# Optimization experiments

Hardware: AMD Instinct MI355X
Metric: run time of the kernel (lower is better)

The kernel has to match this reference:

```python
import jax, jax.numpy as jnp
import numpy as np


def _gru_dir(x, wih, whh, bih, bhh):
    # x: [B, T, Din]; torch GRU gate order is (r, z, n)
    H = whh.shape[-1]
    def step(h, xt):
        gi = xt @ wih.T + bih            # [B, 3H]
        gh = h @ whh.T + bhh             # [B, 3H]
        i_r, i_z, i_n = jnp.split(gi, 3, axis=-1)
        h_r, h_z, h_n = jnp.split(gh, 3, axis=-1)
        r = jax.nn.sigmoid(i_r + h_r)
        z = jax.nn.sigmoid(i_z + h_z)
        n = jnp.tanh(i_n + r * h_n)
        h = (1.0 - z) * n + z * h
        return h, h
    h0 = jnp.zeros((x.shape[0], H), x.dtype)
    _, ys = jax.lax.scan(step, h0, jnp.swapaxes(x, 0, 1))
    return jnp.swapaxes(ys, 0, 1)


def _bigru(x, wih, whh, bih, bhh):
    f = _gru_dir(x, wih[0], whh[0], bih[0], bhh[0])
    b = _gru_dir(x[:, ::-1], wih[1], whh[1], bih[1], bhh[1])[:, ::-1]
    return jnp.concatenate([f, b], axis=-1)


def _masked_max(h, lens):
    # max over first lens[i] timesteps; zeros when lens[i] == 0 (matches max_pool1d loop)
    T = h.shape[1]
    mask = (jnp.arange(T)[None, :] < lens[:, None])[..., None]
    pooled = jnp.max(jnp.where(mask, h, -jnp.inf), axis=1)
    return jnp.where((lens > 0)[:, None], pooled, 0.0)


def _forward(x, events, n_docs, event_tfs, sent_targets, embed,
             word_wih, word_whh, word_bih, word_bhh,
             sent_wih, sent_whh, sent_bih, sent_bhh,
             doc_wih, doc_whh, doc_bih, doc_bhh,
             ev_wih, ev_whh, ev_bih, ev_bhh,
             doc_pos_embed, sent_pos_embed,
             w_event_content, W_event_sal, event_tf, event_sent, event_bias,
             w_sent_content, W_sent_sal, w_sent_doc_pos, w_sent_pos,
             W_event_rel, b_event_rel, event_para, event_zero, sent_bias):
    S, T = x.shape
    spd = S // n_docs                  # sentences per doc (uniform doc_lens)
    eps = events.shape[0] // S         # events per sentence (uniform event_sent_lens)
    sent_lens = jnp.sum(jnp.sign(x), axis=1)
    # embed_frozen=True -> detach embedding output
    xw = jax.lax.stop_gradient(embed[x])               # [S, T, D]
    h = _bigru(xw, word_wih, word_whh, word_bih, word_bhh)  # [S, T, 2H]
    sent_vec = _masked_max(h, sent_lens)               # [S, 2H]
    # sent_RNN per doc (state resets per doc) then full-length max pool
    dh = _bigru(sent_vec.reshape(n_docs, spd, -1), sent_wih, sent_whh, sent_bih, sent_bhh)
    doc_vec = jnp.max(dh, axis=1)                      # [n_docs, 2H]
    bh = _bigru(doc_vec[None], doc_wih, doc_whh, doc_bih, doc_bhh)
    blog_vec = jnp.max(bh[0], axis=0)                  # [2H]
    # teacher_forcing=1.0 -> first-pass sent scores are the detached targets
    sent_probs0 = jax.lax.stop_gradient(sent_targets)
    # events: fixed length 4, full max pool
    eh = _bigru(jax.lax.stop_gradient(embed[events]), ev_wih, ev_whh, ev_bih, ev_bhh)
    event_vec = jnp.max(eh, axis=1)                    # [E, 2H]
    event_sum = jnp.mean(event_vec, axis=0)            # [2H] (avg pool over all events)
    abs_idx = jnp.repeat(jnp.arange(S), eps)           # event -> absolute sentence index
    ec = event_vec @ w_event_content                   # [E]
    es = jnp.einsum('ed,df,f->e', event_vec, W_event_sal, event_sum)
    event_probs = ec + event_tf[0] * event_tfs + event_bias[0] + es + event_sent[0] * sent_probs0[abs_idx]
    event_scores = jax.lax.stop_gradient(event_probs)
    # per-sentence event relevance (Bilinear with bias, dotted with detached scores)
    ev3 = event_vec.reshape(S, eps, -1)
    sc3 = event_scores.reshape(S, eps)
    sim = jnp.einsum('sd,df,sef->se', sent_vec, W_event_rel, ev3) + b_event_rel[0]
    event_rel = event_para[0] * jnp.sum(sim * sc3, axis=1)   # [S]
    doc_idx = jnp.repeat(jnp.arange(n_docs), spd)
    context = jnp.concatenate([jnp.broadcast_to(blog_vec, (S, blog_vec.shape[0])), doc_vec[doc_idx]], axis=1)  # [S, 4H]
    s_content = sent_vec @ w_sent_content
    s_sal = jnp.einsum('sd,df,sf->s', sent_vec, W_sent_sal, context)
    PD = doc_pos_embed.shape[0]
    PS = sent_pos_embed.shape[0]
    dpos = (doc_idx * PD) // n_docs                    # int(i * pos_doc_size / doc_num)
    j_idx = jnp.tile(jnp.arange(spd), n_docs)
    spos = (j_idx * PS) // spd                         # int(j * pos_sent_size / doc_lens[i])
    s_dpos = doc_pos_embed[dpos] @ w_sent_doc_pos
    s_pos = sent_pos_embed[spos] @ w_sent_pos
    sent_out = s_content + s_sal + s_dpos + s_pos + event_rel + sent_bias[0]
    return sent_out, event_probs


def setup_inputs() -> dict:
    key = jax.random.key(0)
    ks = jax.random.split(key, 40)
    V, D, H, P = 50000, 300, 256, 50
    PD, PS = 40, 30
    n_docs, spd, T, eps = 32, 32, 32, 3
    S = n_docs * spd
    E = S * eps
    def rn(k, shape, s=0.05):
        return jax.random.normal(k, shape, jnp.float32) * s
    inp = {}
    inp['x'] = jax.random.randint(ks[0], (S, T), 0, V, jnp.int32)
    inp['events'] = jax.random.randint(ks[1], (E, 4), 1, V, jnp.int32)
    inp['doc_lens'] = jnp.full((n_docs,), spd, jnp.int32)
    inp['event_doc_lens'] = jnp.full((n_docs,), spd * eps, jnp.int32)
    inp['event_sent_lens'] = jnp.full((S,), eps, jnp.int32)
    inp['event_tfs'] = jax.random.uniform(ks[2], (E,), jnp.float32)
    inp['event_targets'] = jax.random.uniform(ks[3], (E,), jnp.float32)
    inp['sent_targets'] = jax.random.uniform(ks[4], (S,), jnp.float32)
    inp['embed'] = rn(ks[5], (V, D), 0.1)
    i = 6
    for name, din in [('word', D), ('sent', 2 * H), ('doc', 2 * H), ('ev', D)]:
        inp[name + '_wih'] = rn(ks[i], (2, 3 * H, din)); i += 1
        inp[name + '_whh'] = rn(ks[i], (2, 3 * H, H)); i += 1
        inp[name + '_bih'] = rn(ks[i], (2, 3 * H)); i += 1
        inp[name + '_bhh'] = rn(ks[i], (2, 3 * H)); i += 1
    inp['doc_pos_embed'] = rn(ks[i], (PD, P), 0.1); i += 1
    inp['sent_pos_embed'] = rn(ks[i], (PS, P), 0.1); i += 1
    inp['w_event_content'] = rn(ks[i], (2 * H,)); i += 1
    inp['W_event_sal'] = rn(ks[i], (2 * H, 2 * H)); i += 1
    inp['event_tf'] = rn(ks[i], (1,)); i += 1
    inp['event_sent'] = rn(ks[i], (1,)); i += 1
    inp['event_bias'] = rn(ks[i], (1,)); i += 1
    inp['w_sent_content'] = rn(ks[i], (2 * H,)); i += 1
    inp['W_sent_sal'] = rn(ks[i], (2 * H, 4 * H)); i += 1
    inp['w_sent_doc_pos'] = rn(ks[i], (P,)); i += 1
    inp['w_sent_pos'] = rn(ks[i], (P,)); i += 1
    inp['W_event_rel'] = rn(ks[i], (2 * H, 2 * H)); i += 1
    inp['b_event_rel'] = rn(ks[i], (1,)); i += 1
    inp['event_para'] = rn(ks[i], (1,)); i += 1
    inp['event_zero'] = rn(ks[i], (1,)); i += 1
    inp['sent_bias'] = rn(ks[i], (1,)); i += 1
    return inp


def reference(x, events, doc_lens, event_doc_lens, event_sent_lens, event_tfs, event_targets, sent_targets, embed,
              word_wih, word_whh, word_bih, word_bhh,
              sent_wih, sent_whh, sent_bih, sent_bhh,
              doc_wih, doc_whh, doc_bih, doc_bhh,
              ev_wih, ev_whh, ev_bih, ev_bhh,
              doc_pos_embed, sent_pos_embed,
              w_event_content, W_event_sal, event_tf, event_sent, event_bias,
              w_sent_content, W_sent_sal, w_sent_doc_pos, w_sent_pos,
              W_event_rel, b_event_rel, event_para, event_zero, sent_bias):
    n_docs = doc_lens.shape[0]
    return _forward(x, events, n_docs, event_tfs, sent_targets, embed,
                    word_wih, word_whh, word_bih, word_bhh,
                    sent_wih, sent_whh, sent_bih, sent_bhh,
                    doc_wih, doc_whh, doc_bih, doc_bhh,
                    ev_wih, ev_whh, ev_bih, ev_bhh,
                    doc_pos_embed, sent_pos_embed,
                    w_event_content, W_event_sal, event_tf, event_sent, event_bias,
                    w_sent_content, W_sent_sal, w_sent_doc_pos, w_sent_pos,
                    W_event_rel, b_event_rel, event_para, event_zero, sent_bias)
```

## Files before the change

kernel.cpp:

```cpp
#include <hip/hip_runtime.h>
#include <hip/hip_bf16.h>
#include <math.h>

typedef __bf16 bf16_t;
typedef __bf16 bf16x8 __attribute__((ext_vector_type(8)));
typedef __bf16 bf16x4 __attribute__((ext_vector_type(4)));
typedef float  f32x4  __attribute__((ext_vector_type(4)));

#define S_TOT 1024
#define T_W   32
#define D_EMB 300
#define KP    320
#define G3    768
#define Hh    256
#define H2    512
#define E_TOT 3072
#define NCANON 33

__device__ __forceinline__ float fsigm(float x) {
  float e = __builtin_amdgcn_exp2f(x * -1.4426950408889634f);
  return __builtin_amdgcn_rcpf(1.f + e);
}
__device__ __forceinline__ float ftanh_(float x) {
  float e = __builtin_amdgcn_exp2f(x * 2.8853900817779268f);
  return 1.f - 2.f * __builtin_amdgcn_rcpf(1.f + e);
}

__global__ void k_detect(const unsigned short* __restrict__ w, int* __restrict__ flag) {
  int lane = threadIdx.x;
  int sane = 0;
  for (int i = lane; i < 256; i += 64) {
    unsigned short v = w[2 * i];
    int ex = (v >> 7) & 0xFF;
    sane += (ex >= 96 && ex <= 134) ? 1 : 0;
  }
  #pragma unroll
  for (int o = 32; o > 0; o >>= 1) sane += __shfl_down(sane, o, 64);
  if (lane == 0) flag[0] = (sane >= 128) ? 1 : 0;
}

struct Canon {
  const void* src[NCANON];
  int off[NCANON + 1];
};
__global__ void k_canon(Canon c, const int* __restrict__ flag, float* __restrict__ dst) {
  int i = blockIdx.x * 256 + threadIdx.x;
  if (i >= c.off[NCANON]) return;
  int seg = 0;
  while (c.off[seg + 1] <= i) ++seg;
  int j = i - c.off[seg];
  dst[i] = flag[0] ? (float)((const bf16_t*)c.src[seg])[j]
                   : ((const float*)c.src[seg])[j];
}

struct PrepArgs {
  const float* whh[4];   bf16_t* pk[4];
  const float* wih2[2];  bf16_t* pw2[2];
  const float* bih4[4];  const float* bhh4[4]; float* bc4[4];
  const float* tsrc[2];  float* tdst[2];
  const int* x; int* lens;
};
__global__ __launch_bounds__(256) void k_prep(PrepArgs a) {
  int b = blockIdx.x, tid = threadIdx.x;
  if (b < 768) {
    int ti = b / 192, lb = b % 192;
    int id = lb * 256 + tid;
    int lane = id & 63;
    int k0 = (id >> 6) & 7;
    int t9 = id >> 9;
    int sl = t9 % 6;
    int wb = t9 / 6;
    int wv = wb & 7;
    int dir = wb >> 3;
    int g = sl >> 1, jt = sl & 1;
    int l16 = lane & 15, quad = lane >> 4;
    int n = g * Hh + wv * 32 + jt * 16 + l16;
    const float* src = a.whh[ti] + ((size_t)dir * G3 + n) * Hh + k0 * 32 + quad * 8;
    bf16_t* dst = a.pk[ti] + (size_t)id * 8;
    #pragma unroll
    for (int i = 0; i < 8; ++i) dst[i] = (bf16_t)src[i];
  } else if (b < 1248) {
    int ti = (b - 768) / 240, lb = (b - 768) % 240;
    int id = lb * 256 + tid;
    int lane = id & 63;
    int su = id >> 6;
    int s  = su % 40;
    int n0 = (su / 40) % 12;
    int dir = su / 480;
    int j = s / 10, k0 = s % 10;
    int l16 = lane & 15, quad = lane >> 4;
    int n = n0 * 64 + j * 16 + l16;
    int c = k0 * 32 + quad * 8;
    const float* src = a.wih2[ti] + ((size_t)dir * G3 + n) * D_EMB + c;
    bf16_t* dst = a.pw2[ti] + (size_t)id * 8;
    #pragma unroll
    for (int i = 0; i < 8; ++i)
      dst[i] = (c + i < D_EMB) ? (bf16_t)src[i] : (bf16_t)0.f;
  } else if (b < 1272) {
    int ti = (b - 1248) / 6, lb = (b - 1248) % 6;
    int i = lb * 256 + tid;
    if (i < 2 * G3) {
      int c = i % G3;
      a.bc4[ti][i] = a.bih4[ti][i] + (c < 2 * Hh ? a.bhh4[ti][i] : 0.f);
    }
  } else if (b < 2808) {
    __shared__ float tile[32][33];
    int lb = b - 1272;
    int which = lb / 768;
    int r = lb % 768;
    int bx = r % 24, by = (r / 24) % 16, d = r / 384;
    const float* w = a.tsrc[which];
    float* out = a.tdst[which];
    int n0 = bx * 32, k0 = by * 32;
    int tx = tid & 31, ty = tid >> 5;
    for (int i = ty; i < 32; i += 8)
      tile[i][tx] = w[((size_t)d * G3 + n0 + i) * H2 + k0 + tx];
    __syncthreads();
    for (int i = ty; i < 32; i += 8)
      out[((size_t)d * H2 + k0 + i) * G3 + n0 + tx] = tile[tx][i];
  } else {
    int s = (b - 2808) * 256 + tid;
    if (s < S_TOT) {
      int c = 0;
      for (int t = 0; t < T_W; ++t) c += (a.x[s * T_W + t] != 0) ? 1 : 0;
      a.lens[s] = c;
    }
  }
}

__device__ __forceinline__ void gib_body(
    const int* __restrict__ toks, const void* __restrict__ embed,
    const bf16_t* __restrict__ wpk_base, const float* __restrict__ bih_base,
    const int* __restrict__ flag, bf16_t* __restrict__ gi_base,
    size_t gi_dstride, int mbase, int bx) {
  __shared__ __align__(16) bf16_t Bt[2][20480];
  int tid = threadIdx.x;
  int wave = tid >> 6, lane = tid & 63;
  int l16 = lane & 15, quad = lane >> 4;
  int m0 = bx * 128;
  int dir = blockIdx.y;
  int isb = flag[0];
  const bf16_t* wpk = wpk_base + (size_t)dir * 245760;
  const float*  bih = bih_base + (size_t)dir * G3;
  bf16_t* gi = gi_base + (size_t)dir * gi_dstride;

  bf16x8 ah[10], al[10];
  {
    int tok = toks[mbase + m0 + wave * 16 + l16];
    if (isb) {
      const bf16_t* er = (const bf16_t*)embed + (size_t)tok * D_EMB;
      #pragma unroll
      for (int k0 = 0; k0 < 10; ++k0) {
        int c = k0 * 32 + quad * 8;
        bf16x8 v = {};
        if (c + 8 <= D_EMB) {
          bf16x4 t0 = *(const bf16x4*)(er + c);
          bf16x4 t1 = *(const bf16x4*)(er + c + 4);
          v[0]=t0[0]; v[1]=t0[1]; v[2]=t0[2]; v[3]=t0[3];
          v[4]=t1[0]; v[5]=t1[1]; v[6]=t1[2]; v[7]=t1[3];
        } else if (c < D_EMB) {
          bf16x4 t0 = *(const bf16x4*)(er + c);
          v[0]=t0[0]; v[1]=t0[1]; v[2]=t0[2]; v[3]=t0[3];
        }
        ah[k0] = v;
        al[k0] = (bf16x8){};
      }
    } else {
      const float* er = (const float*)embed + (size_t)tok * D_EMB;
      #pragma unroll
      for (int k0 = 0; k0 < 10; ++k0) {
        int c = k0 * 32 + quad * 8;
        float v[8];
        #pragma unroll
// ... 50 lines not shown
        for (int j = 0; j < 4; ++j)
          acc[j] = __builtin_amdgcn_mfma_f32_16x16x32_bf16(al[k0], b[j], acc[j], 0, 0, 0);
        #pragma unroll
        for (int j = 0; j < 4; ++j)
          acc[j] = __builtin_amdgcn_mfma_f32_16x16x32_bf16(ah[k0], b[j], acc[j], 0, 0, 0);
      }
    }
    {
      int row0 = m0 + wave * 16 + quad * 4;
      #pragma unroll
      for (int j = 0; j < 4; ++j) {
        int col = n0 * 64 + j * 16 + l16;
        float bb = bih[col];
        #pragma unroll
        for (int rr = 0; rr < 4; ++rr)
          gi[(size_t)(row0 + rr) * G3 + col] = (bf16_t)(acc[j][rr] + bb);
      }
    }
    if (n0 + 1 < 12) {
      bf16_t* dst = &Bt[cur ^ 1][tid * 8];
      #pragma unroll
      for (int i = 0; i < 5; ++i) *(bf16x8*)(dst + i * 4096) = stg[i];
      __syncthreads();
    }
  }
}

__global__ __launch_bounds__(512, 1) void k_giB(
    const int* __restrict__ toks, const void* __restrict__ embed,
    const bf16_t* __restrict__ wpk_base, const float* __restrict__ bih_base,
    const int* __restrict__ flag, bf16_t* __restrict__ gi_base,
    size_t gi_dstride, int mbase) {
  gib_body(toks, embed, wpk_base, bih_base, flag, gi_base, gi_dstride, mbase,
           blockIdx.x);
}

__device__ __forceinline__ void dev_sgemm(
    const float* __restrict__ A, const float* __restrict__ B,
    const float* __restrict__ bias, void* __restrict__ C,
    int M, int N, int K, int obf, int bx, int by) {
  __shared__ float As[32][65];
  __shared__ float Bs[32][65];
  int bm = bx * 64, bn = by * 64;
  int tid = threadIdx.x;
  int tx = tid & 15, ty = tid >> 4;
  float acc[4][4] = {};
  for (int k0 = 0; k0 < K; k0 += 32) {
    for (int i = tid; i < 64 * 32; i += 256) {
      int m = i >> 5, k = i & 31;
      As[k][m] = (bm + m < M) ? A[(size_t)(bm + m) * K + k0 + k] : 0.f;
    }
    for (int i = tid; i < 32 * 64; i += 256) {
      int k = i >> 6, n = i & 63;
      Bs[k][n] = B[(size_t)(k0 + k) * N + bn + n];
    }
    __syncthreads();
    #pragma unroll 8
    for (int k = 0; k < 32; ++k) {
      float a[4], b[4];
      #pragma unroll
      for (int i = 0; i < 4; ++i) a[i] = As[k][ty + i * 16];
      #pragma unroll
      for (int j = 0; j < 4; ++j) b[j] = Bs[k][tx + j * 16];
      #pragma unroll
      for (int i = 0; i < 4; ++i)
        #pragma unroll
        for (int j = 0; j < 4; ++j) acc[i][j] += a[i] * b[j];
    }
    __syncthreads();
  }
  for (int i = 0; i < 4; ++i) {
    int m = bm + ty + i * 16;
    if (m >= M) continue;
    for (int j = 0; j < 4; ++j) {
      int n = bn + tx + j * 16;
      float v = acc[i][j] + (bias ? bias[n] : 0.f);
      if (obf) ((bf16_t*)C)[(size_t)m * N + n] = (bf16_t)v;
      else     ((float*)C)[(size_t)m * N + n] = v;
    }
  }
}

__global__ __launch_bounds__(256) void k_sgemm_su(
    const float* __restrict__ sv, const float* __restrict__ wSt,
    const float* __restrict__ bcS, bf16_t* __restrict__ sgi,
    const float* __restrict__ wer, float* __restrict__ u) {
  int y = blockIdx.y;
  if (y < 12)
    dev_sgemm(sv, wSt, bcS, sgi, 1024, G3, H2, 1, blockIdx.x, y);
  else if (y < 24)
    dev_sgemm(sv, wSt + (size_t)H2 * G3, bcS + G3, sgi + (size_t)S_TOT * G3,
              1024, G3, H2, 1, blockIdx.x, y - 12);
  else
    dev_sgemm(sv, wer, nullptr, u, 1024, H2, H2, 0, blockIdx.x, y - 24);
}

__global__ __launch_bounds__(256) void k_sgemm_d(
    const float* __restrict__ dv, const float* __restrict__ wDt,
    const float* __restrict__ bcD, bf16_t* __restrict__ dgi) {
  int y = blockIdx.y;
  if (y < 12)
    dev_sgemm(dv, wDt, bcD, dgi, 32, G3, H2, 1, 0, y);
  else
    dev_sgemm(dv, wDt + (size_t)H2 * G3, bcD + G3, dgi + (size_t)32 * G3,
              32, G3, H2, 1, 0, y - 12);
}

__device__ __forceinline__ void gru_body(
    const bf16_t* __restrict__ gi, size_t gi_dstride,
    const bf16_t* __restrict__ whhP, const float* __restrict__ bhh,
    const int* __restrict__ lens, float* __restrict__ pool,
    int T, int sbase, int nsent, int sblk) {
  int dir = blockIdx.y;
  int tid = threadIdx.x;
  int wave = tid >> 6, lane = tid & 63;
  int l16 = lane & 15, quad = lane >> 4;
  const bf16_t* giD  = gi + (size_t)dir * gi_dstride;
  const float*  bhhD = bhh + (size_t)dir * G3;

  __shared__ __align__(16) bf16_t hA[2][8][16][4][8];

  bf16x8 Bf[48];
  {
    const bf16_t* Bb = whhP + (size_t)dir * G3 * Hh + (size_t)wave * 48 * 512 + lane * 8;
    #pragma unroll
    for (int s = 0; s < 48; ++s) Bf[s] = *(const bf16x8*)(Bb + s * 512);
  }
  float bhn[2];
  #pragma unroll
  for (int jt = 0; jt < 2; ++jt)
    bhn[jt] = bhhD[2 * Hh + wave * 32 + jt * 16 + l16];
  int Lm[4];
  #pragma unroll
  for (int r = 0; r < 4; ++r) {
    int sa = sblk + quad * 4 + r;
    Lm[r] = (lens && sa < nsent) ? lens[sbase + sa] : T;
  }
  float pmax[2][4], hreg[2][4];
  #pragma unroll
  for (int jt = 0; jt < 2; ++jt)
    #pragma unroll
    for (int r = 0; r < 4; ++r) { pmax[jt][r] = -1e30f; hreg[jt][r] = 0.f; }

  int t0 = dir ? (T - 1) : 0;
  long long stepoff = dir ? -(long long)G3 : (long long)G3;
  const bf16_t* rp[4];
// ... 63 lines not shown
        for (int r = 0; r < 4; ++r) {
          gv[0][jt][r] = rp[r][j];
          gv[1][jt][r] = rp[r][Hh + j];
          gv[2][jt][r] = rp[r][2 * Hh + j];
        }
      }
    }
    asm volatile("s_waitcnt lgkmcnt(0)" ::: "memory");
    __builtin_amdgcn_s_barrier();
    cur ^= 1;
  }
  #pragma unroll
  for (int jt = 0; jt < 2; ++jt) {
    int j = wave * 32 + jt * 16 + l16;
    #pragma unroll
    for (int r = 0; r < 4; ++r) {
      int sa = sblk + quad * 4 + r;
      if (sa < nsent) {
        float v = pmax[jt][r];
        if (v < -9e29f) v = 0.f;
        pool[(size_t)(sbase + sa) * H2 + dir * Hh + j] = v;
      }
    }
  }
}

__global__ __launch_bounds__(512)
__attribute__((amdgpu_waves_per_eu(2, 2)))
void k_gruM(
    const bf16_t* __restrict__ gi, size_t gi_dstride,
    const bf16_t* __restrict__ whhP, const float* __restrict__ bhh,
    const int* __restrict__ lens, float* __restrict__ pool,
    int T, int sbase, int nsent) {
  gru_body(gi, gi_dstride, whhP, bhh, lens, pool, T, sbase, nsent, blockIdx.x * 16);
}

__global__ __launch_bounds__(512)
__attribute__((amdgpu_waves_per_eu(2, 2)))
void k_wg(
    const bf16_t* __restrict__ giW, size_t strideW,
    const bf16_t* __restrict__ whhW, const float* __restrict__ bhhW,
    const int* __restrict__ lens, float* __restrict__ poolW,
    const int* __restrict__ etoks, const void* __restrict__ embed,
    const bf16_t* __restrict__ wpkE, const float* __restrict__ bihE,
    const int* __restrict__ flag, bf16_t* __restrict__ giE, size_t strideE) {
  if ((int)blockIdx.x < 64)
    gru_body(giW, strideW, whhW, bhhW, lens, poolW, 32, 0, 1024,
             blockIdx.x * 16);
  else
    gib_body(etoks, embed, wpkE, bihE, flag, giE, strideE, 0,
             blockIdx.x - 64);
}

__global__ __launch_bounds__(512) void k_colsal(
    const float* __restrict__ ev, float* __restrict__ part,
    const float* __restrict__ W, const float* __restrict__ blog,
    const float* __restrict__ dv, float* __restrict__ wsal) {
  int b = blockIdx.x, t = threadIdx.x;
  if (b < 48) {
    int r0 = b * 64;
    float s = 0.f;
    for (int r = 0; r < 64; ++r) s += ev[(size_t)(r0 + r) * H2 + t];
    part[(size_t)b * H2 + t] = s;
  } else {
    int doc = b - 48;
    const float* row = W + (size_t)t * (2 * H2);
    const float* dvr = dv + (size_t)doc * H2;
    float s = 0.f;
    for (int f = 0; f < H2; ++f) s += row[f] * blog[f];
    for (int f = 0; f < H2; ++f) s += row[H2 + f] * dvr[f];
    wsal[(size_t)doc * H2 + t] = s;
  }
}

__global__ __launch_bounds__(512) void k_esumves(
    const float* __restrict__ part, const float* __restrict__ W,
    float* __restrict__ ves) {
  __shared__ float es[H2];
  int t = threadIdx.x;
  float s = 0.f;
  for (int b = 0; b < 48; ++b) s += part[(size_t)b * H2 + t];
  es[t] = s;
  __syncthreads();
  const float* row = W + (size_t)t * H2;
  float v = 0.f;
  for (int f = 0; f < H2; ++f) v += row[f] * es[f];
  ves[t] = v * (1.f / 3072.f);
}

__global__ __launch_bounds__(256) void k_eventprobs(
    const float* __restrict__ evv, const float* __restrict__ ves,
    const float* __restrict__ w_ec, const float* __restrict__ tfs,
    const float* __restrict__ st, const float* __restrict__ c_tf,
    const float* __restrict__ c_sent, const float* __restrict__ c_bias,
    const int* __restrict__ flag, float* __restrict__ probs, void* __restrict__ outp) {
  int lane = threadIdx.x & 63;
  int e = blockIdx.x * 4 + (threadIdx.x >> 6);
  const float* row = evv + (size_t)e * H2;
  float s = 0.f;
  for (int f = lane; f < H2; f += 64) s += row[f] * (w_ec[f] + ves[f]);
  #pragma unroll
  for (int o = 32; o > 0; o >>= 1) s += __shfl_down(s, o, 64);
  if (lane == 0) {
    float p = s + c_tf[0] * tfs[e] + c_bias[0] + c_sent[0] * st[e / 3];
    probs[e] = p;
    if (flag[0]) ((bf16_t*)outp)[S_TOT + e] = (bf16_t)p;
    else         ((float*)outp)[S_TOT + e] = p;
  }
}

__global__ __launch_bounds__(256) void k_sentout(
    const float* __restrict__ sv, const float* __restrict__ u,
    const float* __restrict__ evv, const float* __restrict__ probs,
    const float* __restrict__ wsal, const float* __restrict__ w_sc,
    const float* __restrict__ dpe, const float* __restrict__ spe,
    const float* __restrict__ w_sdp, const float* __restrict__ w_sp,
    const float* __restrict__ b_rel, const float* __restrict__ para,
    const float* __restrict__ sbias, const int* __restrict__ flag,
    void* __restrict__ outp) {
  int lane = threadIdx.x & 63;
  int s = blockIdx.x * 4 + (threadIdx.x >> 6);
  int doc = s >> 5, jj = s & 31;
  const float* svr = sv + (size_t)s * H2;
  const float* ur  = u + (size_t)s * H2;
  const float* wd  = wsal + (size_t)doc * H2;
  float acc = 0.f, e0 = 0.f, e1 = 0.f, e2 = 0.f;
  for (int f = lane; f < H2; f += 64) {
    float svf = svr[f], uf = ur[f];
    acc += svf * (w_sc[f] + wd[f]);
    e0 += uf * evv[(size_t)(s * 3 + 0) * H2 + f];
    e1 += uf * evv[(size_t)(s * 3 + 1) * H2 + f];
    e2 += uf * evv[(size_t)(s * 3 + 2) * H2 + f];
  }
  if (lane < 50) {
    int dpos = (doc * 40) / 32;
    int spos = (jj * 30) / 32;
    acc += dpe[dpos * 50 + lane] * w_sdp[lane] + spe[spos * 50 + lane] * w_sp[lane];
  }
  #pragma unroll
  for (int o = 32; o > 0; o >>= 1) {
    acc += __shfl_down(acc, o, 64);
    e0  += __shfl_down(e0, o, 64);
    e1  += __shfl_down(e1, o, 64);
    e2  += __shfl_down(e2, o, 64);
  }
  if (lane == 0) {
    float br = b_rel[0];
    float rel = (e0 + br) * probs[s * 3 + 0] + (e1 + br) * probs[s * 3 + 1]
              + (e2 + br) * probs[s * 3 + 2];
    float v = acc + para[0] * rel + sbias[0];
    if (flag[0]) ((bf16_t*)outp)[s] = (bf16_t)v;
    else         ((float*)outp)[s] = v;
  }
}

extern "C" void kernel_launch(void* const* d_in, const int* in_sizes, int n_in,
                              void* d_out, int out_size, void* d_ws, size_t ws_size,
                              hipStream_t stream) {
  (void)in_sizes; (void)n_in; (void)out_size;
  const int* x      = (const int*)d_in[0];
  const int* events = (const int*)d_in[1];
  const void* embed = d_in[8];

  char* ws = (char*)d_ws;
  size_t off = 0;
  auto alloc = [&](size_t bytes) -> void* {
    void* p = ws + off;
    off += (bytes + 255) & ~(size_t)255;
    return p;
  };

  static const int cidx[NCANON] = {9,10,11,12, 13,14,15,16, 17,18,19,20, 21,22,23,24,
                                   25,26,27,28,29,30,31, 32,33,34,35, 36,37,38,40, 5,7};
  static const int csz[NCANON]  = {2*G3*D_EMB, 2*G3*Hh, 2*G3, 2*G3,
                                   2*G3*H2,    2*G3*Hh, 2*G3, 2*G3,
                                   2*G3*H2,    2*G3*Hh, 2*G3, 2*G3,
                                   2*G3*D_EMB, 2*G3*Hh, 2*G3, 2*G3,
                                   40*50, 30*50, H2, H2*H2, 1, 1, 1,
                                   H2, H2*2*H2, 50, 50,
                                   H2*H2, 1, 1, 1, E_TOT, S_TOT};
  Canon cd;
  int tot = 0;
  for (int i = 0; i < NCANON; ++i) { cd.src[i] = d_in[cidx[i]]; cd.off[i] = tot; tot += csz[i]; }
  cd.off[NCANON] = tot;

  int*   flag  = (int*)alloc(256);
  float* canon = (float*)alloc((size_t)tot * 4);
  float* cptr[NCANON];
  for (int i = 0; i < NCANON; ++i) cptr[i] = canon + cd.off[i];
  float *cw_wih = cptr[0], *cw_whh = cptr[1], *cw_bih = cptr[2], *cw_bhh = cptr[3];
  float *cs_wih = cptr[4], *cs_whh = cptr[5], *cs_bih = cptr[6], *cs_bhh = cptr[7];
  float *cd_wih = cptr[8], *cd_whh = cptr[9], *cd_bih = cptr[10], *cd_bhh = cptr[11];
  float *ce_wih = cptr[12], *ce_whh = cptr[13], *ce_bih = cptr[14], *ce_bhh = cptr[15];
  float *c_dpe = cptr[16], *c_spe = cptr[17], *c_wec = cptr[18], *c_Wes = cptr[19];
  float *c_tf = cptr[20], *c_sent = cptr[21], *c_ebias = cptr[22];
  float *c_wsc = cptr[23], *c_Wss = cptr[24], *c_wsdp = cptr[25], *c_wsp = cptr[26];
  float *c_Wer = cptr[27], *c_brel = cptr[28], *c_para = cptr[29], *c_sbias = cptr[30];
  float *c_tfs = cptr[31], *c_starg = cptr[32];

  bf16_t* packW = (bf16_t*)alloc((size_t)2 * G3 * Hh * 2);
  bf16_t* packE = (bf16_t*)alloc((size_t)2 * G3 * Hh * 2);
  bf16_t* packS = (bf16_t*)alloc((size_t)2 * G3 * Hh * 2);
  bf16_t* packD = (bf16_t*)alloc((size_t)2 * G3 * Hh * 2);
  bf16_t* packGiW = (bf16_t*)alloc((size_t)2 * 12 * 40 * 64 * 8 * 2);
  bf16_t* packGiE = (bf16_t*)alloc((size_t)2 * 12 * 40 * 64 * 8 * 2);
  float*  bcW  = (float*)alloc((size_t)2 * G3 * 4);
  float*  bcE  = (float*)alloc((size_t)2 * G3 * 4);
  float*  bcS  = (float*)alloc((size_t)2 * G3 * 4);
  float*  bcD  = (float*)alloc((size_t)2 * G3 * 4);
  float*  sv   = (float*)alloc((size_t)S_TOT * H2 * 4);
  float*  evv  = (float*)alloc((size_t)E_TOT * H2 * 4);
  float*  dv   = (float*)alloc((size_t)32 * H2 * 4);
  float*  blog = (float*)alloc((size_t)H2 * 4);
  float*  wSt  = (float*)alloc((size_t)2 * H2 * G3 * 4);
  float*  wDt  = (float*)alloc((size_t)2 * H2 * G3 * 4);
  float*  u    = (float*)alloc((size_t)S_TOT * H2 * 4);
  float*  part = (float*)alloc((size_t)48 * H2 * 4);
  float*  ves  = (float*)alloc((size_t)H2 * 4);
  float*  wsal = (float*)alloc((size_t)32 * H2 * 4);
  float*  probs= (float*)alloc((size_t)E_TOT * 4);
  int*    lens = (int*)alloc((size_t)S_TOT * 4);
  bf16_t* sgi  = (bf16_t*)alloc((size_t)2 * S_TOT * G3 * 2);
  bf16_t* dgi  = (bf16_t*)alloc((size_t)2 * 32 * G3 * 2);

  size_t fixed = off;
  size_t avail = (ws_size > fixed) ? (ws_size - fixed) : 0;
  const size_t needW = (size_t)2 * 32768 * G3 * 2;
  const size_t needE = (size_t)2 * 12288 * G3 * 2;
  bf16_t* gib = (bf16_t*)(ws + fixed);

  PrepArgs pa;
  pa.whh[0]=cw_whh; pa.whh[1]=ce_whh; pa.whh[2]=cs_whh; pa.whh[3]=cd_whh;
  pa.pk[0]=packW; pa.pk[1]=packE; pa.pk[2]=packS; pa.pk[3]=packD;
  pa.wih2[0]=cw_wih; pa.wih2[1]=ce_wih; pa.pw2[0]=packGiW; pa.pw2[1]=packGiE;
  pa.bih4[0]=cw_bih; pa.bih4[1]=ce_bih; pa.bih4[2]=cs_bih; pa.bih4[3]=cd_bih;
  pa.bhh4[0]=cw_bhh; pa.bhh4[1]=ce_bhh; pa.bhh4[2]=cs_bhh; pa.bhh4[3]=cd_bhh;
  pa.bc4[0]=bcW; pa.bc4[1]=bcE; pa.bc4[2]=bcS; pa.bc4[3]=bcD;
  pa.tsrc[0]=cs_wih; pa.tsrc[1]=cd_wih; pa.tdst[0]=wSt; pa.tdst[1]=wDt;
  pa.x = x; pa.lens = lens;

  k_detect<<<1, 64, 0, stream>>>((const unsigned short*)embed, flag);
  k_canon<<<(tot + 255) / 256, 256, 0, stream>>>(cd, flag, canon);
  k_prep<<<2812, 256, 0, stream>>>(pa);

  if (avail >= needW + needE) {
    bf16_t* egib = (bf16_t*)((char*)gib + ((needW + 255) & ~(size_t)255));
    k_giB<<<dim3(256, 2), 512, 0, stream>>>(x, embed, packGiW, bcW, flag,
                                            gib, (size_t)32768 * G3, 0);
    k_wg<<<dim3(64 + 96, 2), 512, 0, stream>>>(
        gib, (size_t)32768 * G3, packW, cw_bhh, lens, sv,
        events, embed, packGiE, bcE, flag, egib, (size_t)12288 * G3);
    k_gruM<<<dim3(192, 2), 512, 0, stream>>>(
        egib, (size_t)12288 * G3, packE, ce_bhh, nullptr, evv, 4, 0, 3072);
  } else {
    long long rpc = (long long)(avail / ((size_t)G3 * 2 * 2));
    rpc &= ~511LL;
    if (rpc < 512) rpc = 512;
    if (rpc > 32768) rpc = 32768;
    for (long long r0 = 0; r0 < 32768; r0 += rpc) {
      long long rows = 32768 - r0; if (rows > rpc) rows = rpc;
      k_giB<<<dim3((int)(rows / 128), 2), 512, 0, stream>>>(
          x, embed, packGiW, bcW, flag, gib, (size_t)rows * G3, (int)r0);
      k_gruM<<<dim3((int)(rows / 512), 2), 512, 0, stream>>>(
          gib, (size_t)rows * G3, packW, cw_bhh, lens, sv, 32, (int)(r0 / 32),
          (int)(rows / 32));
    }
    for (long long r0 = 0; r0 < 12288; r0 += rpc) {
      long long rows = 12288 - r0; if (rows > rpc) rows = rpc;
      k_giB<<<dim3((int)(rows / 128), 2), 512, 0, stream>>>(
          events, embed, packGiE, bcE, flag, gib, (size_t)rows * G3, (int)r0);
      k_gruM<<<dim3((int)(rows / 64), 2), 512, 0, stream>>>(
          gib, (size_t)rows * G3, packE, ce_bhh, nullptr, evv, 4, (int)(r0 / 4),
          (int)(rows / 4));
    }
  }

  k_sgemm_su<<<dim3(16, 32), 256, 0, stream>>>(sv, wSt, bcS, sgi, c_Wer, u);
  k_gruM<<<dim3(2, 2), 512, 0, stream>>>(sgi, (size_t)S_TOT * G3, packS, cs_bhh,
                                         nullptr, dv, 32, 0, 32);
  k_sgemm_d<<<dim3(1, 24), 256, 0, stream>>>(dv, wDt, bcD, dgi);
  k_gruM<<<dim3(1, 2), 512, 0, stream>>>(dgi, (size_t)32 * G3, packD, cd_bhh,
                                         nullptr, blog, 32, 0, 1);
  k_colsal<<<80, 512, 0, stream>>>(evv, part, c_Wss, blog, dv, wsal);
  k_esumves<<<1, 512, 0, stream>>>(part, c_Wes, ves);
  k_eventprobs<<<768, 256, 0, stream>>>(evv, ves, c_wec, c_tfs, c_starg,
                                        c_tf, c_sent, c_ebias, flag, probs, d_out);
  k_sentout<<<256, 256, 0, stream>>>(sv, u, evv, probs, wsal, c_wsc, c_dpe, c_spe,
                                     c_wsdp, c_wsp, c_brel, c_para, c_sbias, flag, d_out);
}
```

Measured before the change: 913.0 us.

## Fuse tail kernels into combined launches and drop big-weight canonicalization pass

Removes the separate canonicalization kernel for large GRU weights; the prep kernel now reads raw fp32/bf16 inputs directly and handles the small canonical tensors itself. The tail-stage kernels are regrouped so independent work runs in shared launches: the event GRU with the sentence GEMMs, the sentence GRU with the column sums, the doc GEMM with the event-sum projection, and the doc GRU with the event probabilities. This reduces launch count and serialization and lets small, latency-bound stages overlap. The cost is heterogeneous blocks within a launch and forced occupancy hints that may not suit every branch.

```diff
diff --git a/kernel.cpp b/kernel.cpp
--- a/kernel.cpp
+++ b/kernel.cpp
@@ -10,12 +10,11 @@
 #define S_TOT 1024
 #define T_W   32
 #define D_EMB 300
-#define KP    320
 #define G3    768
 #define Hh    256
 #define H2    512
 #define E_TOT 3072
-#define NCANON 33
+#define NC2   21
 
 __device__ __forceinline__ float fsigm(float x) {
   float e = __builtin_amdgcn_exp2f(x * -1.4426950408889634f);
@@ -24,6 +23,9 @@
 __device__ __forceinline__ float ftanh_(float x) {
   float e = __builtin_amdgcn_exp2f(x * 2.8853900817779268f);
   return 1.f - 2.f * __builtin_amdgcn_rcpf(1.f + e);
+}
+__device__ __forceinline__ float ldf(const void* p, size_t i, int isb) {
+  return isb ? (float)((const bf16_t*)p)[i] : ((const float*)p)[i];
 }
 
 __global__ void k_detect(const unsigned short* __restrict__ w, int* __restrict__ flag) {
@@ -40,28 +42,21 @@
 }
 
 struct Canon {
-  const void* src[NCANON];
-  int off[NCANON + 1];
+  const void* src[NC2];
+  int off[NC2 + 1];
 };
-__global__ void k_canon(Canon c, const int* __restrict__ flag, float* __restrict__ dst) {
-  int i = blockIdx.x * 256 + threadIdx.x;
-  if (i >= c.off[NCANON]) return;
-  int seg = 0;
-  while (c.off[seg + 1] <= i) ++seg;
-  int j = i - c.off[seg];
-  dst[i] = flag[0] ? (float)((const bf16_t*)c.src[seg])[j]
-                   : ((const float*)c.src[seg])[j];
-}
-
 struct PrepArgs {
-  const float* whh[4];   bf16_t* pk[4];
-  const float* wih2[2];  bf16_t* pw2[2];
-  const float* bih4[4];  const float* bhh4[4]; float* bc4[4];
-  const float* tsrc[2];  float* tdst[2];
+  const void* whhR[4];  bf16_t* pk[4];
+  const void* wihR[2];  bf16_t* pw2[2];
+  const void* bihR[4];  const void* bhhR[4]; float* bc4[4];
+  const void* tsrcR[2]; float* tdst[2];
   const int* x; int* lens;
+  const int* flag;
+  Canon c; float* canon_dst; int tot2;
 };
-__global__ __launch_bounds__(256) void k_prep(PrepArgs a) {
+__global__ __launch_bounds__(256) void k_prepAll(PrepArgs a) {
   int b = blockIdx.x, tid = threadIdx.x;
+  int isb = a.flag[0];
   if (b < 768) {
     int ti = b / 192, lb = b % 192;
     int id = lb * 256 + tid;
@@ -75,10 +70,10 @@
     int g = sl >> 1, jt = sl & 1;
     int l16 = lane & 15, quad = lane >> 4;
     int n = g * Hh + wv * 32 + jt * 16 + l16;
-    const float* src = a.whh[ti] + ((size_t)dir * G3 + n) * Hh + k0 * 32 + quad * 8;
+    size_t base = ((size_t)dir * G3 + n) * Hh + k0 * 32 + quad * 8;
     bf16_t* dst = a.pk[ti] + (size_t)id * 8;
     #pragma unroll
-    for (int i = 0; i < 8; ++i) dst[i] = (bf16_t)src[i];
+    for (int i = 0; i < 8; ++i) dst[i] = (bf16_t)ldf(a.whhR[ti], base + i, isb);
   } else if (b < 1248) {
     int ti = (b - 768) / 240, lb = (b - 768) % 240;
     int id = lb * 256 + tid;
@@ -91,17 +86,17 @@
     int l16 = lane & 15, quad = lane >> 4;
     int n = n0 * 64 + j * 16 + l16;
     int c = k0 * 32 + quad * 8;
-    const float* src = a.wih2[ti] + ((size_t)dir * G3 + n) * D_EMB + c;
+    size_t base = ((size_t)dir * G3 + n) * D_EMB + c;
     bf16_t* dst = a.pw2[ti] + (size_t)id * 8;
     #pragma unroll
     for (int i = 0; i < 8; ++i)
-      dst[i] = (c + i < D_EMB) ? (bf16_t)src[i] : (bf16_t)0.f;
+      dst[i] = (c + i < D_EMB) ? (bf16_t)ldf(a.wihR[ti], base + i, isb) : (bf16_t)0.f;
   } else if (b < 1272) {
     int ti = (b - 1248) / 6, lb = (b - 1248) % 6;
     int i = lb * 256 + tid;
     if (i < 2 * G3) {
       int c = i % G3;
-      a.bc4[ti][i] = a.bih4[ti][i] + (c < 2 * Hh ? a.bhh4[ti][i] : 0.f);
+      a.bc4[ti][i] = ldf(a.bihR[ti], i, isb) + (c < 2 * Hh ? ldf(a.bhhR[ti], i, isb) : 0.f);
     }
   } else if (b < 2808) {
     __shared__ float tile[32][33];
@@ -109,22 +104,31 @@
     int which = lb / 768;
     int r = lb % 768;
     int bx = r % 24, by = (r / 24) % 16, d = r / 384;
-    const float* w = a.tsrc[which];
+    const void* w = a.tsrcR[which];
     float* out = a.tdst[which];
     int n0 = bx * 32, k0 = by * 32;
     int tx = tid & 31, ty = tid >> 5;
     for (int i = ty; i < 32; i += 8)
-      tile[i][tx] = w[((size_t)d * G3 + n0 + i) * H2 + k0 + tx];
+      tile[i][tx] = ldf(w, ((size_t)d * G3 + n0 + i) * H2 + k0 + tx, isb);
     __syncthreads();
     for (int i = ty; i < 32; i += 8)
       out[((size_t)d * H2 + k0 + i) * G3 + n0 + tx] = tile[tx][i];
-  } else {
+  } else if (b < 2812) {
     int s = (b - 2808) * 256 + tid;
     if (s < S_TOT) {
       int c = 0;
       for (int t = 0; t < T_W; ++t) c += (a.x[s * T_W + t] != 0) ? 1 : 0;
       a.lens[s] = c;
     }
+  } else {
+    int i = (b - 2812) * 256 + tid;
+    if (i < a.tot2) {
+      int seg = 0;
+      while (a.c.off[seg + 1] <= i) ++seg;
+      int j = i - a.c.off[seg];
+      a.canon_dst[i] = isb ? (float)((const bf16_t*)a.c.src[seg])[j]
+                           : ((const float*)a.c.src[seg])[j];
+    }
   }
 }
 
@@ -132,13 +136,12 @@
     const int* __restrict__ toks, const void* __restrict__ embed,
     const bf16_t* __restrict__ wpk_base, const float* __restrict__ bih_base,
     const int* __restrict__ flag, bf16_t* __restrict__ gi_base,
-    size_t gi_dstride, int mbase, int bx) {
+    size_t gi_dstride, int mbase, int bx, int dir) {
   __shared__ __align__(16) bf16_t Bt[2][20480];
   int tid = threadIdx.x;
   int wave = tid >> 6, lane = tid & 63;
   int l16 = lane & 15, quad = lane >> 4;
   int m0 = bx * 128;
-  int dir = blockIdx.y;
   int isb = flag[0];
   const bf16_t* wpk = wpk_base + (size_t)dir * 245760;
   const float*  bih = bih_base + (size_t)dir * G3;
@@ -255,7 +258,7 @@
     const int* __restrict__ flag, bf16_t* __restrict__ gi_base,
     size_t gi_dstride, int mbase) {
   gib_body(toks, embed, wpk_base, bih_base, flag, gi_base, gi_dstride, mbase,
-           blockIdx.x);
+           blockIdx.x, blockIdx.y);
 }
 
 __device__ __forceinline__ void dev_sgemm(
@@ -304,37 +307,61 @@
   }
 }
 
-__global__ __launch_bounds__(256) void k_sgemm_su(
-    const float* __restrict__ sv, const float* __restrict__ wSt,
-    const float* __restrict__ bcS, bf16_t* __restrict__ sgi,
-    const float* __restrict__ wer, float* __restrict__ u) {
-  int y = blockIdx.y;
-  if (y < 12)
-    dev_sgemm(sv, wSt, bcS, sgi, 1024, G3, H2, 1, blockIdx.x, y);
-  else if (y < 24)
-    dev_sgemm(sv, wSt + (size_t)H2 * G3, bcS + G3, sgi + (size_t)S_TOT * G3,
-              1024, G3, H2, 1, blockIdx.x, y - 12);
-  else
-    dev_sgemm(sv, wer, nullptr, u, 1024, H2, H2, 0, blockIdx.x, y - 24);
-}
-
-__global__ __launch_bounds__(256) void k_sgemm_d(
-    const float* __restrict__ dv, const float* __restrict__ wDt,
-    const float* __restrict__ bcD, bf16_t* __restrict__ dgi) {
-  int y = blockIdx.y;
-  if (y < 12)
-    dev_sgemm(dv, wDt, bcD, dgi, 32, G3, H2, 1, 0, y);
-  else
-    dev_sgemm(dv, wDt + (size_t)H2 * G3, bcD + G3, dgi + (size_t)32 * G3,
-              32, G3, H2, 1, 0, y - 12);
+__device__ __forceinline__ void dev_sgemm512(
+    const float* __restrict__ A, const float* __restrict__ B,
+    const float* __restrict__ bias, void* __restrict__ C,
+    int M, int N, int K, int obf, int bx, int by) {
+  __shared__ float As[32][65];
+  __shared__ float Bs[32][65];
+  int bm = bx * 64, bn = by * 64;
+  int tid = threadIdx.x;
+  int tx = tid & 15, ty = (tid >> 4) & 15;
+  float acc[4][4] = {};
+  for (int k0 = 0; k0 < K; k0 += 32) {
+    for (int i = tid; i < 64 * 32; i += 512) {
+      int m = i >> 5, k = i & 31;
+      As[k][m] = (bm + m < M) ? A[(size_t)(bm + m) * K + k0 + k] : 0.f;
+    }
+    for (int i = tid; i < 32 * 64; i += 512) {
+      int k = i >> 6, n = i & 63;
+      Bs[k][n] = B[(size_t)(k0 + k) * N + bn + n];
+    }
+    __syncthreads();
+    if (tid < 256) {
+      #pragma unroll 8
+      for (int k = 0; k < 32; ++k) {
+        float a[4], b[4];
+        #pragma unroll
+        for (int i = 0; i < 4; ++i) a[i] = As[k][ty + i * 16];
+        #pragma unroll
+        for (int j = 0; j < 4; ++j) b[j] = Bs[k][tx + j * 16];
+        #pragma unroll
+        for (int i = 0; i < 4; ++i)
+          #pragma unroll
+          for (int j = 0; j < 4; ++j) acc[i][j] += a[i] * b[j];
+      }
+    }
+    __syncthreads();
+  }
+  if (tid < 256) {
+    for (int i = 0; i < 4; ++i) {
+      int m = bm + ty + i * 16;
+      if (m >= M) continue;
+      for (int j = 0; j < 4; ++j) {
+        int n = bn + tx + j * 16;
+        float v = acc[i][j] + (bias ? bias[n] : 0.f);
+        if (obf) ((bf16_t*)C)[(size_t)m * N + n] = (bf16_t)v;
+        else     ((float*)C)[(size_t)m * N + n] = v;
+      }
+    }
+  }
 }
 
 __device__ __forceinline__ void gru_body(
     const bf16_t* __restrict__ gi, size_t gi_dstride,
     const bf16_t* __restrict__ whhP, const float* __restrict__ bhh,
     const int* __restrict__ lens, float* __restrict__ pool,
-    int T, int sbase, int nsent, int sblk) {
-  int dir = blockIdx.y;
+    int T, int sbase, int nsent, int sblk, int dir) {
   int tid = threadIdx.x;
   int wave = tid >> 6, lane = tid & 63;
   int l16 = lane & 15, quad = lane >> 4;
@@ -464,7 +491,8 @@
     const bf16_t* __restrict__ whhP, const float* __restrict__ bhh,
     const int* __restrict__ lens, float* __restrict__ pool,
     int T, int sbase, int nsent) {
-  gru_body(gi, gi_dstride, whhP, bhh, lens, pool, T, sbase, nsent, blockIdx.x * 16);
+  gru_body(gi, gi_dstride, whhP, bhh, lens, pool, T, sbase, nsent,
+           blockIdx.x * 16, blockIdx.y);
 }
 
 __global__ __launch_bounds__(512)
@@ -478,67 +506,128 @@
     const int* __restrict__ flag, bf16_t* __restrict__ giE, size_t strideE) {
   if ((int)blockIdx.x < 64)
     gru_body(giW, strideW, whhW, bhhW, lens, poolW, 32, 0, 1024,
-             blockIdx.x * 16);
+             blockIdx.x * 16, blockIdx.y);
   else
     gib_body(etoks, embed, wpkE, bihE, flag, giE, strideE, 0,
-             blockIdx.x - 64);
-}
-
-__global__ __launch_bounds__(512) void k_colsal(
-    const float* __restrict__ ev, float* __restrict__ part,
-    const float* __restrict__ W, const float* __restrict__ blog,
-    const float* __restrict__ dv, float* __restrict__ wsal) {
+             blockIdx.x - 64, blockIdx.y);
+}
+
+__global__ __launch_bounds__(512)
+__attribute__((amdgpu_waves_per_eu(2, 2)))
+void k_tail1(
+    const bf16_t* __restrict__ giE, size_t strideE,
+    const bf16_t* __restrict__ packE, const float* __restrict__ bhhE,
+    float* __restrict__ evv,
+    const float* __restrict__ sv, const float* __restrict__ wSt,
+    const float* __restrict__ bcS, bf16_t* __restrict__ sgi,
+    const float* __restrict__ wer, float* __restrict__ u, int evblocks) {
+  int b = blockIdx.x;
+  if (b < evblocks) {
+    int dir = b / 192, bx = b % 192;
+    gru_body(giE, strideE, packE, bhhE, nullptr, evv, 4, 0, 3072, bx * 16, dir);
+  } else {
+    int b2 = b - evblocks;
+    int bx = b2 & 15, y = b2 >> 4;
+    if (y < 12)
+      dev_sgemm512(sv, wSt, bcS, sgi, 1024, G3, H2, 1, bx, y);
+    else if (y < 24)
+      dev_sgemm512(sv, wSt + (size_t)H2 * G3, bcS + G3, sgi + (size_t)S_TOT * G3,
+                   1024, G3, H2, 1, bx, y - 12);
+    else
+      dev_sgemm512(sv, wer, nullptr, u, 1024, H2, H2, 0, bx, y - 24);
+  }
+}
+
+__global__ __launch_bounds__(512)
+__attribute__((amdgpu_waves_per_eu(2, 2)))
+void k_tail2(
+    const bf16_t* __restrict__ sgi, const bf16_t* __restrict__ packS,
+    const float* __restrict__ bhhS, float* __restrict__ dv,
+    const float* __restrict__ evv, float* __restrict__ part) {
   int b = blockIdx.x, t = threadIdx.x;
-  if (b < 48) {
-    int r0 = b * 64;
+  if (b < 4) {
+    gru_body(sgi, (size_t)S_TOT * G3, packS, bhhS, nullptr, dv, 32, 0, 32,
+             (b & 1) * 16, b >> 1);
+  } else {
+    int cb = b - 4;
+    int r0 = cb * 64;
     float s = 0.f;
-    for (int r = 0; r < 64; ++r) s += ev[(size_t)(r0 + r) * H2 + t];
-    part[(size_t)b * H2 + t] = s;
+    for (int r = 0; r < 64; ++r) s += evv[(size_t)(r0 + r) * H2 + t];
+    part[(size_t)cb * H2 + t] = s;
+  }
+}
+
+__global__ __launch_bounds__(256) void k_tail3(
+    const float* __restrict__ dv, const float* __restrict__ wDt,
+    const float* __restrict__ bcD, bf16_t* __restrict__ dgi,
+    const float* __restrict__ part, const float* __restrict__ Wes,
+    float* __restrict__ ves) {
+  int b = blockIdx.x, t = threadIdx.x;
+  if (b < 24) {
+    int y = b;
+    if (y < 12)
+      dev_sgemm(dv, wDt, bcD, dgi, 32, G3, H2, 1, 0, y);
+    else
+      dev_sgemm(dv, wDt + (size_t)H2 * G3, bcD + G3, dgi + (size_t)32 * G3,
+                32, G3, H2, 1, 0, y - 12);
   } else {
-    int doc = b - 48;
-    const float* row = W + (size_t)t * (2 * H2);
-    const float* dvr = dv + (size_t)doc * H2;
-    float s = 0.f;
-    for (int f = 0; f < H2; ++f) s += row[f] * blog[f];
-    for (int f = 0; f < H2; ++f) s += row[H2 + f] * dvr[f];
-    wsal[(size_t)doc * H2 + t] = s;
-  }
-}
-
-__global__ __launch_bounds__(512) void k_esumves(
-    const float* __restrict__ part, const float* __restrict__ W,
-    float* __restrict__ ves) {
-  __shared__ float es[H2];
-  int t = threadIdx.x;
-  float s = 0.f;
-  for (int b = 0; b < 48; ++b) s += part[(size_t)b * H2 + t];
-  es[t] = s;
-  __syncthreads();
-  const float* row = W + (size_t)t * H2;
-  float v = 0.f;
-  for (int f = 0; f < H2; ++f) v += row[f] * es[f];
-  ves[t] = v * (1.f / 3072.f);
-}
-
-__global__ __launch_bounds__(256) void k_eventprobs(
+    __shared__ float es[H2];
+    for (int c = t; c < H2; c += 256) {
+      float s = 0.f;
+      for (int bb = 0; bb < 48; ++bb) s += part[(size_t)bb * H2 + c];
+      es[c] = s;
+    }
+    __syncthreads();
+    for (int r = t; r < H2; r += 256) {
+      const float* row = Wes + (size_t)r * H2;
+      float v = 0.f;
+      for (int f = 0; f < H2; ++f) v += row[f] * es[f];
+      ves[r] = v * (1.f / 3072.f);
+    }
+  }
+}
+
+__global__ __launch_bounds__(512)
+__attribute__((amdgpu_waves_per_eu(2, 2)))
+void k_tail4(
+    const bf16_t* __restrict__ dgi, const bf16_t* __restrict__ packD,
+    const float* __restrict__ bhhD, float* __restrict__ blog,
     const float* __restrict__ evv, const float* __restrict__ ves,
     const float* __restrict__ w_ec, const float* __restrict__ tfs,
     const float* __restrict__ st, const float* __restrict__ c_tf,
     const float* __restrict__ c_sent, const float* __restrict__ c_bias,
-    const int* __restrict__ flag, float* __restrict__ probs, void* __restrict__ outp) {
-  int lane = threadIdx.x & 63;
-  int e = blockIdx.x * 4 + (threadIdx.x >> 6);
-  const float* row = evv + (size_t)e * H2;
+    const int* __restrict__ flag, float* __restrict__ probs,
+    void* __restrict__ outp) {
+  int b = blockIdx.x;
+  if (b < 2) {
+    gru_body(dgi, (size_t)32 * G3, packD, bhhD, nullptr, blog, 32, 0, 1, 0, b);
+  } else {
+    int lane = threadIdx.x & 63;
+    int e = (b - 2) * 8 + (threadIdx.x >> 6);
+    const float* row = evv + (size_t)e * H2;
+    float s = 0.f;
+    for (int f = lane; f < H2; f += 64) s += row[f] * (w_ec[f] + ves[f]);
+    #pragma unroll
+    for (int o = 32; o > 0; o >>= 1) s += __shfl_down(s, o, 64);
+    if (lane == 0) {
+      float p = s + c_tf[0] * tfs[e] + c_bias[0] + c_sent[0] * st[e / 3];
+      probs[e] = p;
+      if (flag[0]) ((bf16_t*)outp)[S_TOT + e] = (bf16_t)p;
+      else         ((float*)outp)[S_TOT + e] = p;
+    }
+  }
+}
+
+__global__ __launch_bounds__(512) void k_tail5(
+    const float* __restrict__ W, const float* __restrict__ blog,
+    const float* __restrict__ dv, float* __restrict__ wsal) {
+  int doc = blockIdx.x, t = threadIdx.x;
+  const float* row = W + (size_t)t * (2 * H2);
+  const float* dvr = dv + (size_t)doc * H2;
   float s = 0.f;
-  for (int f = lane; f < H2; f += 64) s += row[f] * (w_ec[f] + ves[f]);
-  #pragma unroll
-  for (int o = 32; o > 0; o >>= 1) s += __shfl_down(s, o, 64);
-  if (lane == 0) {
-    float p = s + c_tf[0] * tfs[e] + c_bias[0] + c_sent[0] * st[e / 3];
-    probs[e] = p;
-    if (flag[0]) ((bf16_t*)outp)[S_TOT + e] = (bf16_t)p;
-    else         ((float*)outp)[S_TOT + e] = p;
-  }
+  for (int f = 0; f < H2; ++f) s += row[f] * blog[f];
+  for (int f = 0; f < H2; ++f) s += row[H2 + f] * dvr[f];
+  wsal[(size_t)doc * H2 + t] = s;
 }
 
 __global__ __launch_bounds__(256) void k_sentout(
@@ -602,33 +691,27 @@
     return p;
   };
 
-  static const int cidx[NCANON] = {9,10,11,12, 13,14,15,16, 17,18,19,20, 21,22,23,24,
-                                   25,26,27,28,29,30,31, 32,33,34,35, 36,37,38,40, 5,7};
-  static const int csz[NCANON]  = {2*G3*D_EMB, 2*G3*Hh, 2*G3, 2*G3,
-                                   2*G3*H2,    2*G3*Hh, 2*G3, 2*G3,
-                                   2*G3*H2,    2*G3*Hh, 2*G3, 2*G3,
-                                   2*G3*D_EMB, 2*G3*Hh, 2*G3, 2*G3,
-                                   40*50, 30*50, H2, H2*H2, 1, 1, 1,
-                                   H2, H2*2*H2, 50, 50,
-                                   H2*H2, 1, 1, 1, E_TOT, S_TOT};
+  static const int cidx[NC2] = {12,16,20,24, 25,26,27,28,29,30,31,
+                                32,33,34,35,36,37,38,40, 5,7};
+  static const int csz[NC2]  = {2*G3, 2*G3, 2*G3, 2*G3,
+                                40*50, 30*50, H2, H2*H2, 1, 1, 1,
+                                H2, H2*2*H2, 50, 50, H2*H2, 1, 1, 1,
+                                E_TOT, S_TOT};
   Canon cd;
-  int tot = 0;
-  for (int i = 0; i < NCANON; ++i) { cd.src[i] = d_in[cidx[i]]; cd.off[i] = tot; tot += csz[i]; }
-  cd.off[NCANON] = tot;
+  int tot2 = 0;
+  for (int i = 0; i < NC2; ++i) { cd.src[i] = d_in[cidx[i]]; cd.off[i] = tot2; tot2 += csz[i]; }
+  cd.off[NC2] = tot2;
 
   int*   flag  = (int*)alloc(256);
-  float* canon = (float*)alloc((size_t)tot * 4);
-  float* cptr[NCANON];
-  for (int i = 0; i < NCANON; ++i) cptr[i] = canon + cd.off[i];
-  float *cw_wih = cptr[0], *cw_whh = cptr[1], *cw_bih = cptr[2], *cw_bhh = cptr[3];
-  float *cs_wih = cptr[4], *cs_whh = cptr[5], *cs_bih = cptr[6], *cs_bhh = cptr[7];
-  float *cd_wih = cptr[8], *cd_whh = cptr[9], *cd_bih = cptr[10], *cd_bhh = cptr[11];
-  float *ce_wih = cptr[12], *ce_whh = cptr[13], *ce_bih = cptr[14], *ce_bhh = cptr[15];
-  float *c_dpe = cptr[16], *c_spe = cptr[17], *c_wec = cptr[18], *c_Wes = cptr[19];
-  float *c_tf = cptr[20], *c_sent = cptr[21], *c_ebias = cptr[22];
-  float *c_wsc = cptr[23], *c_Wss = cptr[24], *c_wsdp = cptr[25], *c_wsp = cptr[26];
-  float *c_Wer = cptr[27], *c_brel = cptr[28], *c_para = cptr[29], *c_sbias = cptr[30];
-  float *c_tfs = cptr[31], *c_starg = cptr[32];
+  float* canon = (float*)alloc((size_t)tot2 * 4);
+  float* cptr[NC2];
+  for (int i = 0; i < NC2; ++i) cptr[i] = canon + cd.off[i];
+  float *cw_bhh = cptr[0], *cs_bhh = cptr[1], *cd_bhh = cptr[2], *ce_bhh = cptr[3];
+  float *c_dpe = cptr[4], *c_spe = cptr[5], *c_wec = cptr[6], *c_Wes = cptr[7];
+  float *c_tf = cptr[8], *c_sent = cptr[9], *c_ebias = cptr[10];
+  float *c_wsc = cptr[11], *c_Wss = cptr[12], *c_wsdp = cptr[13], *c_wsp = cptr[14];
+  float *c_Wer = cptr[15], *c_brel = cptr[16], *c_para = cptr[17], *c_sbias = cptr[18];
+  float *c_tfs = cptr[19], *c_starg = cptr[20];
 
   bf16_t* packW = (bf16_t*)alloc((size_t)2 * G3 * Hh * 2);
   bf16_t* packE = (bf16_t*)alloc((size_t)2 * G3 * Hh * 2);
@@ -662,18 +745,20 @@
   bf16_t* gib = (bf16_t*)(ws + fixed);
 
   PrepArgs pa;
-  pa.whh[0]=cw_whh; pa.whh[1]=ce_whh; pa.whh[2]=cs_whh; pa.whh[3]=cd_whh;
+  pa.whhR[0]=d_in[10]; pa.whhR[1]=d_in[22]; pa.whhR[2]=d_in[14]; pa.whhR[3]=d_in[18];
   pa.pk[0]=packW; pa.pk[1]=packE; pa.pk[2]=packS; pa.pk[3]=packD;
-  pa.wih2[0]=cw_wih; pa.wih2[1]=ce_wih; pa.pw2[0]=packGiW; pa.pw2[1]=packGiE;
-  pa.bih4[0]=cw_bih; pa.bih4[1]=ce_bih; pa.bih4[2]=cs_bih; pa.bih4[3]=cd_bih;
-  pa.bhh4[0]=cw_bhh; pa.bhh4[1]=ce_bhh; pa.bhh4[2]=cs_bhh; pa.bhh4[3]=cd_bhh;
+  pa.wihR[0]=d_in[9]; pa.wihR[1]=d_in[21]; pa.pw2[0]=packGiW; pa.pw2[1]=packGiE;
+  pa.bihR[0]=d_in[11]; pa.bihR[1]=d_in[23]; pa.bihR[2]=d_in[15]; pa.bihR[3]=d_in[19];
+  pa.bhhR[0]=d_in[12]; pa.bhhR[1]=d_in[24]; pa.bhhR[2]=d_in[16]; pa.bhhR[3]=d_in[20];
   pa.bc4[0]=bcW; pa.bc4[1]=bcE; pa.bc4[2]=bcS; pa.bc4[3]=bcD;
-  pa.tsrc[0]=cs_wih; pa.tsrc[1]=cd_wih; pa.tdst[0]=wSt; pa.tdst[1]=wDt;
+  pa.tsrcR[0]=d_in[13]; pa.tsrcR[1]=d_in[17]; pa.tdst[0]=wSt; pa.tdst[1]=wDt;
   pa.x = x; pa.lens = lens;
+  pa.flag = flag; pa.c = cd; pa.canon_dst = canon; pa.tot2 = tot2;
+
+  int prepBlocks = 2812 + (tot2 + 255) / 256;
 
   k_detect<<<1, 64, 0, stream>>>((const unsigned short*)embed, flag);
-  k_canon<<<(tot + 255) / 256, 256, 0, stream>>>(cd, flag, canon);
-  k_prep<<<2812, 256, 0, stream>>>(pa);
+  k_prepAll<<<prepBlocks, 256, 0, stream>>>(pa);
 
   if (avail >= needW + needE) {
     bf16_t* egib = (bf16_t*)((char*)gib + ((needW + 255) & ~(size_t)255));
@@ -682,8 +767,9 @@
     k_wg<<<dim3(64 + 96, 2), 512, 0, stream>>>(
         gib, (size_t)32768 * G3, packW, cw_bhh, lens, sv,
         events, embed, packGiE, bcE, flag, egib, (size_t)12288 * G3);
-    k_gruM<<<dim3(192, 2), 512, 0, stream>>>(
-        egib, (size_t)12288 * G3, packE, ce_bhh, nullptr, evv, 4, 0, 3072);
+    k_tail1<<<384 + 512, 512, 0, stream>>>(
+        egib, (size_t)12288 * G3, packE, ce_bhh, evv,
+        sv, wSt, bcS, sgi, c_Wer, u, 384);
   } else {
     long long rpc = (long long)(avail / ((size_t)G3 * 2 * 2));
     rpc &= ~511LL;
@@ -705,18 +791,16 @@
           gib, (size_t)rows * G3, packE, ce_bhh, nullptr, evv, 4, (int)(r0 / 4),
           (int)(rows / 4));
     }
-  }
-
-  k_sgemm_su<<<dim3(16, 32), 256, 0, stream>>>(sv, wSt, bcS, sgi, c_Wer, u);
-  k_gruM<<<dim3(2, 2), 512, 0, stream>>>(sgi, (size_t)S_TOT * G3, packS, cs_bhh,
-                                         nullptr, dv, 32, 0, 32);
-  k_sgemm_d<<<dim3(1, 24), 256, 0, stream>>>(dv, wDt, bcD, dgi);
-  k_gruM<<<dim3(1, 2), 512, 0, stream>>>(dgi, (size_t)32 * G3, packD, cd_bhh,
-                                         nullptr, blog, 32, 0, 1);
-  k_colsal<<<80, 512, 0, stream>>>(evv, part, c_Wss, blog, dv, wsal);
-  k_esumves<<<1, 512, 0, stream>>>(part, c_Wes, ves);
-  k_eventprobs<<<768, 256, 0, stream>>>(evv, ves, c_wec, c_tfs, c_starg,
-                                        c_tf, c_sent, c_ebias, flag, probs, d_out);
+    k_tail1<<<512, 512, 0, stream>>>(
+        nullptr, 0, packE, ce_bhh, evv, sv, wSt, bcS, sgi, c_Wer, u, 0);
+  }
+
+  k_tail2<<<52, 512, 0, stream>>>(sgi, packS, cs_bhh, dv, evv, part);
+  k_tail3<<<25, 256, 0, stream>>>(dv, wDt, bcD, dgi, part, c_Wes, ves);
+  k_tail4<<<386, 512, 0, stream>>>(dgi, packD, cd_bhh, blog, evv, ves,
+                                   c_wec, c_tfs, c_starg, c_tf, c_sent, c_ebias,
+                                   flag, probs, d_out);
+  k_tail5<<<32, 512, 0, stream>>>(c_Wss, blog, dv, wsal);
   k_sentout<<<256, 256, 0, stream>>>(sv, u, evv, probs, wsal, c_wsc, c_dpe, c_spe,
                                      c_wsdp, c_wsp, c_brel, c_para, c_sbias, flag, d_out);
 }
```

Result: faster. 865.6 us (-5.2%).
